# Kernel tuning notes

Hardware: AMD Instinct MI355X
Metric: run time of the kernel (lower is better)

## Reference

```python
import jax, jax.numpy as jnp
import numpy as np

N_ENT, N_REL, D = 20000, 500, 200
B, K = 8, 16


def setup_inputs() -> dict:
    key = jax.random.key(0)
    ks = jax.random.split(key, 24)
    inp = {}
    inp["batch"] = jax.random.randint(ks[0], (B, K, 3), 0, N_REL, dtype=jnp.int64 if jax.config.jax_enable_x64 else jnp.int32)
    inp["eemb"] = jax.random.normal(ks[1], (N_ENT, 2 * D), jnp.float32)
    inp["remb"] = jax.random.normal(ks[2], (N_REL, D), jnp.float32)
    inp["ce_re"] = jax.random.normal(ks[3], (N_ENT, D), jnp.float32)
    inp["ce_im"] = jax.random.normal(ks[4], (N_ENT, D), jnp.float32)
    inp["cr_re"] = jax.random.normal(ks[5], (N_REL, D), jnp.float32)
    inp["cr_im"] = jax.random.normal(ks[6], (N_REL, D), jnp.float32)
    inp["de"] = jax.random.normal(ks[7], (N_ENT, D), jnp.float32)
    inp["dr"] = jax.random.normal(ks[8], (N_REL, D), jnp.float32)
    inp["ke"] = jax.random.normal(ks[9], (N_ENT, D), jnp.float32)
    inp["kr"] = jax.random.normal(ks[10], (N_REL, D), jnp.float32)
    inp["se_h"] = jax.random.normal(ks[11], (N_ENT, D), jnp.float32)
    inp["se_t"] = jax.random.normal(ks[12], (N_ENT, D), jnp.float32)
    inp["sr"] = jax.random.normal(ks[13], (N_REL, D), jnp.float32)
    inp["sr_inv"] = jax.random.normal(ks[14], (N_REL, D), jnp.float32)
    # gate MLP params, stacked over 5 experts; uniform(0, 0.1) like cfg.model.init
    inp["W0"] = jax.random.uniform(ks[15], (5, 10, 64), jnp.float32) * 0.1
    inp["b0"] = jnp.zeros((5, 64), jnp.float32)
    inp["W1"] = jax.random.uniform(ks[16], (5, 64, 64), jnp.float32) * 0.1
    inp["b1"] = jnp.zeros((5, 64), jnp.float32)
    inp["W2"] = jax.random.uniform(ks[17], (5, 64, 64), jnp.float32) * 0.1
    inp["b2"] = jnp.zeros((5, 64), jnp.float32)
    inp["W3"] = jax.random.uniform(ks[18], (5, 64, 1), jnp.float32) * 0.1
    inp["b3"] = jnp.zeros((5, 1), jnp.float32)
    return inp


def _features_and_normalize(score):
    # min-max normalize per row, then summary features (eval mode: keep full row)
    mn = jnp.min(score, axis=1, keepdims=True)
    s = score - mn
    mx = jnp.max(s, axis=1, keepdims=True)
    s = s / mx
    mean = jnp.mean(s, axis=1, keepdims=True)
    var = jnp.var(s, axis=1, ddof=1, keepdims=True)  # torch.var default: unbiased
    return s, 1.0 - mean, var


def _forward(batch, eemb, remb, ce_re, ce_im, cr_re, cr_im, de, dr, ke, kr,
             se_h, se_t, sr, sr_inv, W0, b0, W1, b1, W2, b2, W3, b3):
    h = batch[:, 0, 0]  # h_index[:, 0]
    r = batch[:, 0, 2]  # r_index[:, 0]

    # --- RotatE: gather h, rotate by relation phase, broadcast diff vs full table
    d = remb.shape[1]
    he = eemb[h]                                  # [B, 2d]
    h_re, h_im = he[:, :d], he[:, d:]
    phase = remb[r]                               # [B, d]
    c, s_ = jnp.cos(phase), jnp.sin(phase)
    p_re = h_re * c - h_im * s_
    p_im = h_re * s_ + h_im * c
    t_re, t_im = eemb[:, :d], eemb[:, d:]         # [N, d]
    dre = p_re[:, None, :] - t_re[None]           # [B, N, d]
    dim = p_im[:, None, :] - t_im[None]
    rotate_score = -jnp.sqrt(dre * dre + dim * dim).sum(axis=-1)  # [B, N]

    # --- ComplEx: Re(<h, r, conj(t)>) against full table
    s_re = ce_re[h] * cr_re[r] - ce_im[h] * cr_im[r]
    s_im = ce_re[h] * cr_im[r] + ce_im[h] * cr_re[r]
    complex_score = s_re @ ce_re.T + s_im @ ce_im.T

    # --- KDG / DistMult / SimplE (bilinear diag scores vs full table)
    kdg_score = (ke[h] * kr[r]) @ ke.T
    distmult_score = (de[h] * dr[r]) @ de.T
    simple_score = 0.5 * ((se_h[h] * sr[r]) @ se_t.T + (se_t[h] * sr_inv[r]) @ se_h.T)

    scores, feats = [], []
    for sc in (rotate_score, complex_score, kdg_score, distmult_score, simple_score):
        ns, mdiffs, var = _features_and_normalize(sc)
        scores.append(ns)
        feats += [mdiffs, var]
    mlp_in = jnp.concatenate(feats, axis=1)       # [B, 10]

    # --- per-expert gate MLPs: Linear, Linear+ReLU, Linear+ReLU, Linear(1)+ReLU
    x = jnp.einsum('bi,eio->ebo', mlp_in, W0) + b0[:, None, :]
    x = jax.nn.relu(jnp.einsum('ebi,eio->ebo', x, W1) + b1[:, None, :])
    x = jax.nn.relu(jnp.einsum('ebi,eio->ebo', x, W2) + b2[:, None, :])
    w = jax.nn.relu(jnp.einsum('ebi,eio->ebo', x, W3) + b3[:, None, :])  # [5, B, 1]
    weights = w[:, :, 0].T                        # [B, 5]
    weights = weights / jnp.max(jnp.abs(weights), axis=1, keepdims=True)

    stacked = jnp.stack(scores, axis=1)           # [B, 5, N]
    return jnp.sum(weights[:, :, None] * stacked, axis=1)  # [B, N]


def reference(batch, eemb, remb, ce_re, ce_im, cr_re, cr_im, de, dr, ke, kr,
              se_h, se_t, sr, sr_inv, W0, b0, W1, b1, W2, b2, W3, b3):
    return _forward(batch, eemb, remb, ce_re, ce_im, cr_re, cr_im, de, dr, ke, kr,
                    se_h, se_t, sr, sr_inv, W0, b0, W1, b1, W2, b2, W3, b3)
```

## Files before the change

kernel.cpp:

```cpp
#include <hip/hip_runtime.h>
#include <math.h>

#define N_ENT 20000
#define D 200
#define NB 8
#define NM 5
#define NBLK_MAIN 1250

#define Q_OFF     0
#define PART_OFF  12800
#define MNMX_OFF  212800
#define STATD_OFF 212880
#define C_OFF     213040
#define CONST_OFF 213080
#define S_OFF     213088

#define COMP(v,j) ((j)==0 ? (v).x : (j)==1 ? (v).y : (j)==2 ? (v).z : (v).w)
#define LD4(p) (*(const float4*)(p))

__global__ __launch_bounds__(256) void k_q(
    const int* __restrict__ batch, const float* __restrict__ eemb,
    const float* __restrict__ remb,
    const float* __restrict__ ce_re, const float* __restrict__ ce_im,
    const float* __restrict__ cr_re, const float* __restrict__ cr_im,
    const float* __restrict__ de, const float* __restrict__ dr,
    const float* __restrict__ ke, const float* __restrict__ kr,
    const float* __restrict__ se_h, const float* __restrict__ se_t,
    const float* __restrict__ sr, const float* __restrict__ sr_inv,
    float* __restrict__ ws)
{
    int b = blockIdx.x;
    int d = threadIdx.x;
    if (d >= D) return;
    int h = batch[b*48 + 0];
    int r = batch[b*48 + 2];
    float* q = ws + Q_OFF;

    float her = eemb[h*400 + d];
    float hei = eemb[h*400 + 200 + d];
    float ph  = remb[r*200 + d];
    float cph = cosf(ph), sph = sinf(ph);
    q[(0*8 + b)*200 + d] = her*cph - hei*sph;
    q[(1*8 + b)*200 + d] = her*sph + hei*cph;

    float cer = ce_re[h*200+d], cei = ce_im[h*200+d];
    float crr = cr_re[r*200+d], cri = cr_im[r*200+d];
    q[(2*8 + b)*200 + d] = cer*crr - cei*cri;
    q[(3*8 + b)*200 + d] = cer*cri + cei*crr;

    q[(4*8 + b)*200 + d] = ke[h*200+d] * kr[r*200+d];
    q[(5*8 + b)*200 + d] = de[h*200+d] * dr[r*200+d];
    q[(6*8 + b)*200 + d] = se_h[h*200+d] * sr[r*200+d];
    q[(7*8 + b)*200 + d] = se_t[h*200+d] * sr_inv[r*200+d];
}

__global__ __launch_bounds__(256, 3) void k_main(
    const float* __restrict__ eemb, const float* __restrict__ ce_re,
    const float* __restrict__ ce_im, const float* __restrict__ ke,
    const float* __restrict__ de, const float* __restrict__ se_h,
    const float* __restrict__ se_t, float* __restrict__ ws)
{
    __shared__ __align__(16) float ebuf[2][8][16][32];
    __shared__ __align__(16) float qbuf[2][8][8][32];
    __shared__ float4 red2[2][40];

    const float* qg = ws + Q_OFF;
    float* S    = ws + S_OFF;
    float* part = ws + PART_OFF;

    const int tid = threadIdx.x;
    const int wv  = tid >> 6;
    const int l   = tid & 63;
    const int bg  = tid & 3;
    const int rg  = (tid >> 2) & 7;
    const int ds  = tid >> 5;
    const int e0  = blockIdx.x * 16;

    const float *gb0, *gb1; int gs0, go0, gs1, go1;
    switch (wv) {
        case 0: gb0 = eemb;  gs0 = 400; go0 = 0; gb1 = eemb;  gs1 = 400; go1 = 200; break;
        case 1: gb0 = ce_re; gs0 = 200; go0 = 0; gb1 = ce_im; gs1 = 200; go1 = 0;   break;
        case 2: gb0 = ke;    gs0 = 200; go0 = 0; gb1 = de;    gs1 = 200; go1 = 0;   break;
        default:gb0 = se_t;  gs0 = 200; go0 = 0; gb1 = se_h;  gs1 = 200; go1 = 0;   break;
    }
    const int sl = l & 7;
    const int rl = l >> 3;

    auto stage = [&](int buf, int c) {
#pragma unroll
        for (int a = 0; a < 2; ++a) {
            const float* gbase = a ? gb1 : gb0;
            const int gs_ = a ? gs1 : gs0, go_ = a ? go1 : go0;
#pragma unroll
            for (int i = 0; i < 2; ++i) {
                int rr  = i*8 + rl;
                int col = c*32 + ((sl ^ (rr & 7)) << 2);
                if (col + 4 > 200) col = 0;
                const float* gp = gbase + (size_t)(e0 + rr) * gs_ + go_ + col;
                float* lp = &ebuf[buf][2*wv + a][i*8][0];
                __builtin_amdgcn_global_load_lds(
                    (const __attribute__((address_space(1))) void*)gp,
                    (__attribute__((address_space(3))) void*)lp, 16, 0, 0);
            }
        }
#pragma unroll
        for (int a = 0; a < 2; ++a) {
            int v   = 2*wv + a;
            int col = c*32 + ((sl ^ rl) << 2);
            if (col + 4 > 200) col = 0;
            const float* gp = qg + (size_t)(v*8 + rl) * 200 + col;
            float* lp = &qbuf[buf][v][0][0];
            __builtin_amdgcn_global_load_lds(
                (const __attribute__((address_space(1))) void*)gp,
                (__attribute__((address_space(3))) void*)lp, 16, 0, 0);
        }
    };

    float acc[NM][2][2];
#pragma unroll
    for (int m = 0; m < NM; ++m)
#pragma unroll
        for (int je = 0; je < 2; ++je)
#pragma unroll
            for (int jb = 0; jb < 2; ++jb) acc[m][je][jb] = 0.f;

    const int eA = 2*rg, eB = 2*rg + 1;
    const int bA = 2*bg, bB = 2*bg + 1;
    const int peA = ((ds ^ (eA & 7)) << 2), peB = ((ds ^ (eB & 7)) << 2);
    const int pqA = ((ds ^ bA) << 2),       pqB = ((ds ^ bB) << 2);

    stage(0, 0);
    for (int c = 0; c < 7; ++c) {
        __syncthreads();
        if (c < 6) stage((c+1)&1, c+1);
        if (c*32 + ds*4 < 200) {
            const float* eb = &ebuf[c&1][0][0][0];
            const float* qb = &qbuf[c&1][0][0][0];
#define ELOAD(arr, pe, e) LD4(eb + (((arr)*16 + (e))*32) + (pe))
#define QLOAD(v, pq, b)   LD4(qb + (((v)*8 + (b))*32) + (pq))
            {
                float4 q0A=QLOAD(0,pqA,bA), q0B=QLOAD(0,pqB,bB);
                float4 q1A=QLOAD(1,pqA,bA), q1B=QLOAD(1,pqB,bB);
                float4 t0A=ELOAD(0,peA,eA), t0B=ELOAD(0,peB,eB);
                float4 t1A=ELOAD(1,peA,eA), t1B=ELOAD(1,peB,eB);
#pragma unroll
                for (int k = 0; k < 4; ++k) {
                    float dr_, di_;
                    dr_=COMP(q0A,k)-COMP(t0A,k); di_=COMP(q1A,k)-COMP(t1A,k);
                    acc[0][0][0] += __builtin_amdgcn_sqrtf(fmaf(dr_,dr_,di_*di_));
                    dr_=COMP(q0B,k)-COMP(t0A,k); di_=COMP(q1B,k)-COMP(t1A,k);
                    acc[0][0][1] += __builtin_amdgcn_sqrtf(fmaf(dr_,dr_,di_*di_));
                    dr_=COMP(q0A,k)-COMP(t0B,k); di_=COMP(q1A,k)-COMP(t1B,k);
                    acc[0][1][0] += __builtin_amdgcn_sqrtf(fmaf(dr_,dr_,di_*di_));
                    dr_=COMP(q0B,k)-COMP(t0B,k); di_=COMP(q1B,k)-COMP(t1B,k);
                    acc[0][1][1] += __builtin_amdgcn_sqrtf(fmaf(dr_,dr_,di_*di_));
                }
            }
            {
                float4 q2A=QLOAD(2,pqA,bA), q2B=QLOAD(2,pqB,bB);
                float4 q3A=QLOAD(3,pqA,bA), q3B=QLOAD(3,pqB,bB);
                float4 c0A=ELOAD(2,peA,eA), c0B=ELOAD(2,peB,eB);
                float4 c1A=ELOAD(3,peA,eA), c1B=ELOAD(3,peB,eB);
#pragma unroll
                for (int k = 0; k < 4; ++k) {
                    acc[1][0][0]=fmaf(COMP(q2A,k),COMP(c0A,k),fmaf(COMP(q3A,k),COMP(c1A,k),acc[1][0][0]));
                    acc[1][0][1]=fmaf(COMP(q2B,k),COMP(c0A,k),fmaf(COMP(q3B,k),COMP(c1A,k),acc[1][0][1]));
                    acc[1][1][0]=fmaf(COMP(q2A,k),COMP(c0B,k),fmaf(COMP(q3A,k),COMP(c1B,k),acc[1][1][0]));
                    acc[1][1][1]=fmaf(COMP(q2B,k),COMP(c0B,k),fmaf(COMP(q3B,k),COMP(c1B,k),acc[1][1][1]));
                }
            }
            {
                float4 q4A=QLOAD(4,pqA,bA), q4B=QLOAD(4,pqB,bB);
                float4 k0A=ELOAD(4,peA,eA), k0B=ELOAD(4,peB,eB);
                float4 q5A=QLOAD(5,pqA,bA), q5B=QLOAD(5,pqB,bB);
                float4 d0A=ELOAD(5,peA,eA), d0B=ELOAD(5,peB,eB);
#pragma unroll
                for (int k = 0; k < 4; ++k) {
                    acc[2][0][0]=fmaf(COMP(q4A,k),COMP(k0A,k),acc[2][0][0]);
                    acc[2][0][1]=fmaf(COMP(q4B,k),COMP(k0A,k),acc[2][0][1]);
                    acc[2][1][0]=fmaf(COMP(q4A,k),COMP(k0B,k),acc[2][1][0]);
                    acc[2][1][1]=fmaf(COMP(q4B,k),COMP(k0B,k),acc[2][1][1]);
                    acc[3][0][0]=fmaf(COMP(q5A,k),COMP(d0A,k),acc[3][0][0]);
                    acc[3][0][1]=fmaf(COMP(q5B,k),COMP(d0A,k),acc[3][0][1]);
                    acc[3][1][0]=fmaf(COMP(q5A,k),COMP(d0B,k),acc[3][1][0]);
                    acc[3][1][1]=fmaf(COMP(q5B,k),COMP(d0B,k),acc[3][1][1]);
                }
            }
            {
                float4 q6A=QLOAD(6,pqA,bA), q6B=QLOAD(6,pqB,bB);
                float4 q7A=QLOAD(7,pqA,bA), q7B=QLOAD(7,pqB,bB);
                float4 s0A=ELOAD(6,peA,eA), s0B=ELOAD(6,peB,eB);
                float4 s1A=ELOAD(7,peA,eA), s1B=ELOAD(7,peB,eB);
#pragma unroll
                for (int k = 0; k < 4; ++k) {
                    acc[4][0][0]=fmaf(COMP(q6A,k),COMP(s0A,k),fmaf(COMP(q7A,k),COMP(s1A,k),acc[4][0][0]));
                    acc[4][0][1]=fmaf(COMP(q6B,k),COMP(s0A,k),fmaf(COMP(q7B,k),COMP(s1A,k),acc[4][0][1]));
                    acc[4][1][0]=fmaf(COMP(q6A,k),COMP(s0B,k),fmaf(COMP(q7A,k),COMP(s1B,k),acc[4][1][0]));
                    acc[4][1][1]=fmaf(COMP(q6B,k),COMP(s0B,k),fmaf(COMP(q7B,k),COMP(s1B,k),acc[4][1][1]));
                }
            }
        }
    }

    __syncthreads();
    float* ov = &ebuf[0][0][0][0];
    {
        int base = tid * 20;
#pragma unroll
        for (int m = 0; m < NM; ++m)
#pragma unroll
            for (int je = 0; je < 2; ++je)
#pragma unroll
                for (int jb = 0; jb < 2; ++jb)
                    ov[base + m*4 + je*2 + jb] = acc[m][je][jb];
    }
    __syncthreads();
    if (tid < 128) {
        int e_l = tid >> 3, b = tid & 7;
        int rg2 = e_l >> 1, je = e_l & 1, bg2 = b >> 1, jb = b & 1;
        float vals[NM];
#pragma unroll
        for (int m = 0; m < NM; ++m) {
            float s = 0.f;
#pragma unroll
            for (int d2 = 0; d2 < 8; ++d2)
                s += ov[((d2 << 5) | (rg2 << 2) | bg2) * 20 + m*4 + je*2 + jb];
            vals[m] = s;
        }
        vals[0] = -vals[0];
        vals[4] = 0.5f * vals[4];
        int e = e0 + e_l;
#pragma unroll
        for (int m = 0; m < NM; ++m) S[(m*8 + b)*N_ENT + e] = vals[m];

        float mn[NM], mx[NM], sm[NM], sq[NM];
#pragma unroll
        for (int m = 0; m < NM; ++m) {
            mn[m] = vals[m]; mx[m] = vals[m]; sm[m] = vals[m]; sq[m] = vals[m]*vals[m];
        }
#pragma unroll
        for (int off = 8; off <= 32; off <<= 1) {
#pragma unroll
            for (int m = 0; m < NM; ++m) {
                mn[m] = fminf(mn[m], __shfl_xor(mn[m], off, 64));
                mx[m] = fmaxf(mx[m], __shfl_xor(mx[m], off, 64));
                sm[m] += __shfl_xor(sm[m], off, 64);
                sq[m] += __shfl_xor(sq[m], off, 64);
            }
        }
        if ((tid & 63) < 8) {
#pragma unroll
            for (int m = 0; m < NM; ++m)
                red2[tid >> 6][m*8 + b] = make_float4(mn[m], mx[m], sm[m], sq[m]);
        }
    }
    __syncthreads();
    if (tid < 40) {
        float4 u = red2[0][tid], v = red2[1][tid];
        float4 o;
        o.x = fminf(u.x, v.x);
        o.y = fmaxf(u.y, v.y);
        o.z = u.z + v.z;
        o.w = u.w + v.w;
        *(float4*)(part + (blockIdx.x*40 + tid)*4) = o;
    }
}

__global__ __launch_bounds__(256) void k_red(float* __restrict__ ws)
{
    const float* part = ws + PART_OFF;
    const int p = blockIdx.x;
    const int t = threadIdx.x;
    __shared__ float  smn[4], smx[4];
    __shared__ double ssm[4], ssq[4];

    float mn = INFINITY, mx = -INFINITY;
    double sm = 0.0, sq = 0.0;
    for (int blk = t; blk < NBLK_MAIN; blk += 256) {
        float4 v = LD4(part + (blk*40 + p)*4);
        mn = fminf(mn, v.x); mx = fmaxf(mx, v.y);
        sm += (double)v.z;   sq += (double)v.w;
    }
#pragma unroll
    for (int off = 1; off < 64; off <<= 1) {
        mn = fminf(mn, __shfl_xor(mn, off, 64));
        mx = fmaxf(mx, __shfl_xor(mx, off, 64));
        sm += __shfl_xor(sm, off, 64);
        sq += __shfl_xor(sq, off, 64);
    }
    if ((t & 63) == 0) {
        smn[t >> 6] = mn; smx[t >> 6] = mx; ssm[t >> 6] = sm; ssq[t >> 6] = sq;
    }
    __syncthreads();
    if (t == 0) {
        mn = fminf(fminf(smn[0], smn[1]), fminf(smn[2], smn[3]));
        mx = fmaxf(fmaxf(smx[0], smx[1]), fmaxf(smx[2], smx[3]));
        sm = ssm[0] + ssm[1] + ssm[2] + ssm[3];
        sq = ssq[0] + ssq[1] + ssq[2] + ssq[3];
        ws[MNMX_OFF + p*2]     = mn;
        ws[MNMX_OFF + p*2 + 1] = mx;
        double* sd = (double*)(ws + STATD_OFF);
        sd[p*2]     = sm;
        sd[p*2 + 1] = sq;
    }
}

__global__ __launch_bounds__(320) void k_mlp(
    const float* __restrict__ W0, const float* __restrict__ b0,
    const float* __restrict__ W1, const float* __restrict__ b1,
    const float* __restrict__ W2, const float* __restrict__ b2,
    const float* __restrict__ W3, const float* __restrict__ b3,
    float* __restrict__ ws)
{
    __shared__ float feat[NB][10];
    __shared__ float mnS[NM][NB], rngS[NM][NB];
    __shared__ float xA[NM][NB][64], xB[NM][NB][64];
    __shared__ float wS[NM][NB];

    int t = threadIdx.x;
    if (t < 40) {
        int m = t / 8, b = t % 8;
        float  mn = ws[MNMX_OFF + t*2];
        float  mx = ws[MNMX_OFF + t*2 + 1];
        const double* sd = (const double*)(ws + STATD_OFF);
        double sm = sd[t*2], sq = sd[t*2 + 1];
        float  rng  = mx - mn;
        double mean = sm / (double)N_ENT;
        float  md   = 1.0f - (float)((mean - (double)mn) / (double)rng);
        double va   = (sq - sm*sm/(double)N_ENT) / (double)(N_ENT - 1);
        float  vn   = (float)(va / ((double)rng * (double)rng));
        feat[b][2*m]   = md;
        feat[b][2*m+1] = vn;
        mnS[m][b] = mn; rngS[m][b] = rng;
    }
    __syncthreads();

    int ex = t / 64, o = t % 64;
    for (int b = 0; b < NB; ++b) {
        float a = b0[ex*64 + o];
#pragma unroll
        for (int i = 0; i < 10; ++i) a = fmaf(feat[b][i], W0[ex*640 + i*64 + o], a);
        xA[ex][b][o] = a;
    }
    __syncthreads();
    for (int b = 0; b < NB; ++b) {
        float a = b1[ex*64 + o];
        for (int i = 0; i < 64; ++i) a = fmaf(xA[ex][b][i], W1[ex*4096 + i*64 + o], a);
        xB[ex][b][o] = fmaxf(a, 0.f);
    }
    __syncthreads();
    for (int b = 0; b < NB; ++b) {
        float a = b2[ex*64 + o];
        for (int i = 0; i < 64; ++i) a = fmaf(xB[ex][b][i], W2[ex*4096 + i*64 + o], a);
        xA[ex][b][o] = fmaxf(a, 0.f);
    }
    __syncthreads();
    if (o == 0) {
        for (int b = 0; b < NB; ++b) {
            float a = b3[ex];
            for (int i = 0; i < 64; ++i) a = fmaf(xA[ex][b][i], W3[ex*64 + i], a);
            wS[ex][b] = fmaxf(a, 0.f);
        }
    }
    __syncthreads();
    if (t < 8) {
        int b = t;
        float wm = 0.f;
        for (int m = 0; m < NM; ++m) wm = fmaxf(wm, fabsf(wS[m][b]));
        float cst = 0.f;
        for (int m = 0; m < NM; ++m) {
            float w  = wS[m][b] / wm;
            float cc = w / rngS[m][b];
            ws[C_OFF + m*8 + b] = cc;
            cst -= cc * mnS[m][b];
        }
        ws[CONST_OFF + b] = cst;
    }
}

__global__ __launch_bounds__(256) void k_comb(const float* __restrict__ ws,
                                              float* __restrict__ out)
{
    int t = blockIdx.x * 256 + threadIdx.x;
    if (t >= NB * (N_ENT/4)) return;
    int b = t / (N_ENT/4);
    int e = (t % (N_ENT/4)) * 4;
    const float* S = ws + S_OFF;
    float c0 = ws[C_OFF +  0 + b], c1 = ws[C_OFF +  8 + b], c2 = ws[C_OFF + 16 + b];
    float c3 = ws[C_OFF + 24 + b], c4 = ws[C_OFF + 32 + b];
    float cst = ws[CONST_OFF + b];
    float4 s0 = *(const float4*)(S + (0*8 + b)*N_ENT + e);
    float4 s1 = *(const float4*)(S + (1*8 + b)*N_ENT + e);
    float4 s2 = *(const float4*)(S + (2*8 + b)*N_ENT + e);
    float4 s3 = *(const float4*)(S + (3*8 + b)*N_ENT + e);
    float4 s4 = *(const float4*)(S + (4*8 + b)*N_ENT + e);
    float4 o4;
    o4.x = fmaf(c0,s0.x, fmaf(c1,s1.x, fmaf(c2,s2.x, fmaf(c3,s3.x, fmaf(c4,s4.x, cst)))));
    o4.y = fmaf(c0,s0.y, fmaf(c1,s1.y, fmaf(c2,s2.y, fmaf(c3,s3.y, fmaf(c4,s4.y, cst)))));
    o4.z = fmaf(c0,s0.z, fmaf(c1,s1.z, fmaf(c2,s2.z, fmaf(c3,s3.z, fmaf(c4,s4.z, cst)))));
    o4.w = fmaf(c0,s0.w, fmaf(c1,s1.w, fmaf(c2,s2.w, fmaf(c3,s3.w, fmaf(c4,s4.w, cst)))));
    *(float4*)(out + b*N_ENT + e) = o4;
}

extern "C" void kernel_launch(void* const* d_in, const int* in_sizes, int n_in,
                              void* d_out, int out_size, void* d_ws, size_t ws_size,
                              hipStream_t stream)
{
    const int*   batch  = (const int*)  d_in[0];
    const float* eemb   = (const float*)d_in[1];
    const float* remb   = (const float*)d_in[2];
    const float* ce_re  = (const float*)d_in[3];
    const float* ce_im  = (const float*)d_in[4];
    const float* cr_re  = (const float*)d_in[5];
    const float* cr_im  = (const float*)d_in[6];
    const float* de     = (const float*)d_in[7];
    const float* dr     = (const float*)d_in[8];
    const float* ke     = (const float*)d_in[9];
    const float* kr     = (const float*)d_in[10];
    const float* se_h   = (const float*)d_in[11];
    const float* se_t   = (const float*)d_in[12];
    const float* sr     = (const float*)d_in[13];
    const float* sr_inv = (const float*)d_in[14];
    const float* W0 = (const float*)d_in[15];
    const float* b0 = (const float*)d_in[16];
    const float* W1 = (const float*)d_in[17];
    const float* b1 = (const float*)d_in[18];
    const float* W2 = (const float*)d_in[19];
    const float* b2 = (const float*)d_in[20];
    const float* W3 = (const float*)d_in[21];
    const float* b3 = (const float*)d_in[22];
    float* ws  = (float*)d_ws;
    float* out = (float*)d_out;

    k_q    <<<8, 256, 0, stream>>>(batch, eemb, remb, ce_re, ce_im, cr_re, cr_im,
                                   de, dr, ke, kr, se_h, se_t, sr, sr_inv, ws);
    k_main <<<NBLK_MAIN, 256, 0, stream>>>(eemb, ce_re, ce_im, ke, de, se_h, se_t, ws);
    k_red  <<<40, 256, 0, stream>>>(ws);
    k_mlp  <<<1, 320, 0, stream>>>(W0, b0, W1, b1, W2, b2, W3, b3, ws);
    k_comb <<<(NB*(N_ENT/4) + 255)/256, 256, 0, stream>>>(ws, out);
}
```

Before: 63.39 us.

## Load entity rows directly from global, stage only queries in LDS, wave-shuffle reductions

```diff
diff --git a/kernel.cpp b/kernel.cpp
--- a/kernel.cpp
+++ b/kernel.cpp
@@ -54,62 +54,38 @@
     q[(7*8 + b)*200 + d] = se_t[h*200+d] * sr_inv[r*200+d];
 }
 
-__global__ __launch_bounds__(256, 3) void k_main(
+__global__ __launch_bounds__(256, 4) void k_main(
     const float* __restrict__ eemb, const float* __restrict__ ce_re,
     const float* __restrict__ ce_im, const float* __restrict__ ke,
     const float* __restrict__ de, const float* __restrict__ se_h,
     const float* __restrict__ se_t, float* __restrict__ ws)
 {
-    __shared__ __align__(16) float ebuf[2][8][16][32];
-    __shared__ __align__(16) float qbuf[2][8][8][32];
-    __shared__ float4 red2[2][40];
+    __shared__ __align__(16) float qbuf[2][64][32];
 
     const float* qg = ws + Q_OFF;
     float* S    = ws + S_OFF;
     float* part = ws + PART_OFF;
 
     const int tid = threadIdx.x;
-    const int wv  = tid >> 6;
+    const int bg  = tid >> 6;
     const int l   = tid & 63;
-    const int bg  = tid & 3;
-    const int rg  = (tid >> 2) & 7;
-    const int ds  = tid >> 5;
+    const int ds  = (tid >> 3) & 7;
+    const int rg  = tid & 7;
     const int e0  = blockIdx.x * 16;
 
-    const float *gb0, *gb1; int gs0, go0, gs1, go1;
-    switch (wv) {
-        case 0: gb0 = eemb;  gs0 = 400; go0 = 0; gb1 = eemb;  gs1 = 400; go1 = 200; break;
-        case 1: gb0 = ce_re; gs0 = 200; go0 = 0; gb1 = ce_im; gs1 = 200; go1 = 0;   break;
-        case 2: gb0 = ke;    gs0 = 200; go0 = 0; gb1 = de;    gs1 = 200; go1 = 0;   break;
-        default:gb0 = se_t;  gs0 = 200; go0 = 0; gb1 = se_h;  gs1 = 200; go1 = 0;   break;
-    }
-    const int sl = l & 7;
-    const int rl = l >> 3;
-
-    auto stage = [&](int buf, int c) {
-#pragma unroll
-        for (int a = 0; a < 2; ++a) {
-            const float* gbase = a ? gb1 : gb0;
-            const int gs_ = a ? gs1 : gs0, go_ = a ? go1 : go0;
-#pragma unroll
-            for (int i = 0; i < 2; ++i) {
-                int rr  = i*8 + rl;
-                int col = c*32 + ((sl ^ (rr & 7)) << 2);
-                if (col + 4 > 200) col = 0;
-                const float* gp = gbase + (size_t)(e0 + rr) * gs_ + go_ + col;
-                float* lp = &ebuf[buf][2*wv + a][i*8][0];
-                __builtin_amdgcn_global_load_lds(
-                    (const __attribute__((address_space(1))) void*)gp,
-                    (__attribute__((address_space(3))) void*)lp, 16, 0, 0);
-            }
-        }
-#pragma unroll
-        for (int a = 0; a < 2; ++a) {
-            int v   = 2*wv + a;
-            int col = c*32 + ((sl ^ rl) << 2);
-            if (col + 4 > 200) col = 0;
-            const float* gp = qg + (size_t)(v*8 + rl) * 200 + col;
-            float* lp = &qbuf[buf][v][0][0];
+    const int eA = e0 + 2*rg, eB = eA + 1;
+    const int bA = 2*bg,      bB = bA + 1;
+
+    const int r0 = bg*16;
+    const int sr_ = l & 7;
+    const int rr_ = l >> 3;
+
+    auto stage_q = [&](int buf, int c) {
+#pragma unroll
+        for (int i = 0; i < 2; ++i) {
+            int row = r0 + i*8;
+            const float* gp = qg + (size_t)(row + rr_) * 200 + c*32 + (sr_ << 2);
+            float* lp = &qbuf[buf][row][0];
             __builtin_amdgcn_global_load_lds(
                 (const __attribute__((address_space(1))) void*)gp,
                 (__attribute__((address_space(3))) void*)lp, 16, 0, 0);
@@ -124,25 +100,22 @@
 #pragma unroll
             for (int jb = 0; jb < 2; ++jb) acc[m][je][jb] = 0.f;
 
-    const int eA = 2*rg, eB = 2*rg + 1;
-    const int bA = 2*bg, bB = 2*bg + 1;
-    const int peA = ((ds ^ (eA & 7)) << 2), peB = ((ds ^ (eB & 7)) << 2);
-    const int pqA = ((ds ^ bA) << 2),       pqB = ((ds ^ bB) << 2);
-
-    stage(0, 0);
+    stage_q(0, 0);
     for (int c = 0; c < 7; ++c) {
         __syncthreads();
-        if (c < 6) stage((c+1)&1, c+1);
-        if (c*32 + ds*4 < 200) {
-            const float* eb = &ebuf[c&1][0][0][0];
-            const float* qb = &qbuf[c&1][0][0][0];
-#define ELOAD(arr, pe, e) LD4(eb + (((arr)*16 + (e))*32) + (pe))
-#define QLOAD(v, pq, b)   LD4(qb + (((v)*8 + (b))*32) + (pq))
+        if (c < 6) stage_q((c+1)&1, c+1);
+        const int off = c*32 + ds*4;
+        if (off < 200) {
+            const float* qb = &qbuf[c&1][0][0];
+            const int dq = ds << 2;
+#define QLOAD(v, b)  LD4(qb + (((v)*8 + (b)) << 5) + dq)
             {
-                float4 q0A=QLOAD(0,pqA,bA), q0B=QLOAD(0,pqB,bB);
-                float4 q1A=QLOAD(1,pqA,bA), q1B=QLOAD(1,pqB,bB);
-                float4 t0A=ELOAD(0,peA,eA), t0B=ELOAD(0,peB,eB);
-                float4 t1A=ELOAD(1,peA,eA), t1B=ELOAD(1,peB,eB);
+                float4 q0A=QLOAD(0,bA), q0B=QLOAD(0,bB);
+                float4 q1A=QLOAD(1,bA), q1B=QLOAD(1,bB);
+                float4 t0A=LD4(eemb + (size_t)eA*400 + off);
+                float4 t0B=LD4(eemb + (size_t)eB*400 + off);
+                float4 t1A=LD4(eemb + (size_t)eA*400 + 200 + off);
+                float4 t1B=LD4(eemb + (size_t)eB*400 + 200 + off);
 #pragma unroll
                 for (int k = 0; k < 4; ++k) {
                     float dr_, di_;
@@ -157,10 +130,12 @@
                 }
             }
             {
-                float4 q2A=QLOAD(2,pqA,bA), q2B=QLOAD(2,pqB,bB);
-                float4 q3A=QLOAD(3,pqA,bA), q3B=QLOAD(3,pqB,bB);
-                float4 c0A=ELOAD(2,peA,eA), c0B=ELOAD(2,peB,eB);
-                float4 c1A=ELOAD(3,peA,eA), c1B=ELOAD(3,peB,eB);
+                float4 q2A=QLOAD(2,bA), q2B=QLOAD(2,bB);
+                float4 q3A=QLOAD(3,bA), q3B=QLOAD(3,bB);
+                float4 c0A=LD4(ce_re + (size_t)eA*200 + off);
+                float4 c0B=LD4(ce_re + (size_t)eB*200 + off);
+                float4 c1A=LD4(ce_im + (size_t)eA*200 + off);
+                float4 c1B=LD4(ce_im + (size_t)eB*200 + off);
 #pragma unroll
                 for (int k = 0; k < 4; ++k) {
                     acc[1][0][0]=fmaf(COMP(q2A,k),COMP(c0A,k),fmaf(COMP(q3A,k),COMP(c1A,k),acc[1][0][0]));
@@ -170,10 +145,12 @@
                 }
             }
             {
-                float4 q4A=QLOAD(4,pqA,bA), q4B=QLOAD(4,pqB,bB);
-                float4 k0A=ELOAD(4,peA,eA), k0B=ELOAD(4,peB,eB);
-                float4 q5A=QLOAD(5,pqA,bA), q5B=QLOAD(5,pqB,bB);
-                float4 d0A=ELOAD(5,peA,eA), d0B=ELOAD(5,peB,eB);
+                float4 q4A=QLOAD(4,bA), q4B=QLOAD(4,bB);
+                float4 k0A=LD4(ke + (size_t)eA*200 + off);
+                float4 k0B=LD4(ke + (size_t)eB*200 + off);
+                float4 q5A=QLOAD(5,bA), q5B=QLOAD(5,bB);
+                float4 d0A=LD4(de + (size_t)eA*200 + off);
+                float4 d0B=LD4(de + (size_t)eB*200 + off);
 #pragma unroll
                 for (int k = 0; k < 4; ++k) {
                     acc[2][0][0]=fmaf(COMP(q4A,k),COMP(k0A,k),acc[2][0][0]);
@@ -187,10 +164,12 @@
                 }
             }
             {
-                float4 q6A=QLOAD(6,pqA,bA), q6B=QLOAD(6,pqB,bB);
-                float4 q7A=QLOAD(7,pqA,bA), q7B=QLOAD(7,pqB,bB);
-                float4 s0A=ELOAD(6,peA,eA), s0B=ELOAD(6,peB,eB);
-                float4 s1A=ELOAD(7,peA,eA), s1B=ELOAD(7,peB,eB);
+                float4 q6A=QLOAD(6,bA), q6B=QLOAD(6,bB);
+                float4 s0A=LD4(se_t + (size_t)eA*200 + off);
+                float4 s0B=LD4(se_t + (size_t)eB*200 + off);
+                float4 q7A=QLOAD(7,bA), q7B=QLOAD(7,bB);
+                float4 s1A=LD4(se_h + (size_t)eA*200 + off);
+                float4 s1B=LD4(se_h + (size_t)eB*200 + off);
 #pragma unroll
                 for (int k = 0; k < 4; ++k) {
                     acc[4][0][0]=fmaf(COMP(q6A,k),COMP(s0A,k),fmaf(COMP(q7A,k),COMP(s1A,k),acc[4][0][0]));
@@ -202,67 +181,70 @@
         }
     }
 
-    __syncthreads();
-    float* ov = &ebuf[0][0][0][0];
-    {
-        int base = tid * 20;
+#pragma unroll
+    for (int off2 = 8; off2 <= 32; off2 <<= 1)
 #pragma unroll
         for (int m = 0; m < NM; ++m)
 #pragma unroll
             for (int je = 0; je < 2; ++je)
 #pragma unroll
                 for (int jb = 0; jb < 2; ++jb)
-                    ov[base + m*4 + je*2 + jb] = acc[m][je][jb];
-    }
-    __syncthreads();
-    if (tid < 128) {
-        int e_l = tid >> 3, b = tid & 7;
-        int rg2 = e_l >> 1, je = e_l & 1, bg2 = b >> 1, jb = b & 1;
-        float vals[NM];
-#pragma unroll
-        for (int m = 0; m < NM; ++m) {
-            float s = 0.f;
-#pragma unroll
-            for (int d2 = 0; d2 < 8; ++d2)
-                s += ov[((d2 << 5) | (rg2 << 2) | bg2) * 20 + m*4 + je*2 + jb];
-            vals[m] = s;
-        }
-        vals[0] = -vals[0];
-        vals[4] = 0.5f * vals[4];
-        int e = e0 + e_l;
-#pragma unroll
-        for (int m = 0; m < NM; ++m) S[(m*8 + b)*N_ENT + e] = vals[m];
-
-        float mn[NM], mx[NM], sm[NM], sq[NM];
-#pragma unroll
-        for (int m = 0; m < NM; ++m) {
-            mn[m] = vals[m]; mx[m] = vals[m]; sm[m] = vals[m]; sq[m] = vals[m]*vals[m];
-        }
-#pragma unroll
-        for (int off = 8; off <= 32; off <<= 1) {
-#pragma unroll
-            for (int m = 0; m < NM; ++m) {
-                mn[m] = fminf(mn[m], __shfl_xor(mn[m], off, 64));
-                mx[m] = fmaxf(mx[m], __shfl_xor(mx[m], off, 64));
-                sm[m] += __shfl_xor(sm[m], off, 64);
-                sq[m] += __shfl_xor(sq[m], off, 64);
-            }
-        }
-        if ((tid & 63) < 8) {
-#pragma unroll
-            for (int m = 0; m < NM; ++m)
-                red2[tid >> 6][m*8 + b] = make_float4(mn[m], mx[m], sm[m], sq[m]);
-        }
-    }
-    __syncthreads();
-    if (tid < 40) {
-        float4 u = red2[0][tid], v = red2[1][tid];
-        float4 o;
-        o.x = fminf(u.x, v.x);
-        o.y = fmaxf(u.y, v.y);
-        o.z = u.z + v.z;
-        o.w = u.w + v.w;
-        *(float4*)(part + (blockIdx.x*40 + tid)*4) = o;
+                    acc[m][je][jb] += __shfl_xor(acc[m][je][jb], off2, 64);
+
+    float vals[NM][2][2];
+#pragma unroll
+    for (int m = 0; m < NM; ++m)
+#pragma unroll
+        for (int je = 0; je < 2; ++je)
+#pragma unroll
+            for (int jb = 0; jb < 2; ++jb) {
+                float v = acc[m][je][jb];
+                if (m == 0) v = -v;
+                if (m == 4) v = 0.5f * v;
+                vals[m][je][jb] = v;
+            }
+
+#pragma unroll
+    for (int m = 0; m < NM; ++m) {
+        if (ds == m) {
+            S[(m*8 + bA)*N_ENT + eA] = vals[m][0][0];
+            S[(m*8 + bA)*N_ENT + eB] = vals[m][1][0];
+            S[(m*8 + bB)*N_ENT + eA] = vals[m][0][1];
+            S[(m*8 + bB)*N_ENT + eB] = vals[m][1][1];
+        }
+    }
+
+    float mn2[NM][2], mx2[NM][2], sm2[NM][2], sq2[NM][2];
+#pragma unroll
+    for (int m = 0; m < NM; ++m)
+#pragma unroll
+        for (int jb = 0; jb < 2; ++jb) {
+            float a = vals[m][0][jb], b = vals[m][1][jb];
+            mn2[m][jb] = fminf(a, b);
+            mx2[m][jb] = fmaxf(a, b);
+            sm2[m][jb] = a + b;
+            sq2[m][jb] = fmaf(a, a, b*b);
+        }
+#pragma unroll
+    for (int off2 = 1; off2 <= 4; off2 <<= 1)
+#pragma unroll
+        for (int m = 0; m < NM; ++m)
+#pragma unroll
+            for (int jb = 0; jb < 2; ++jb) {
+                mn2[m][jb] = fminf(mn2[m][jb], __shfl_xor(mn2[m][jb], off2, 64));
+                mx2[m][jb] = fmaxf(mx2[m][jb], __shfl_xor(mx2[m][jb], off2, 64));
+                sm2[m][jb] += __shfl_xor(sm2[m][jb], off2, 64);
+                sq2[m][jb] += __shfl_xor(sq2[m][jb], off2, 64);
+            }
+#pragma unroll
+    for (int m = 0; m < NM; ++m) {
+        if (ds == m && rg == 0) {
+#pragma unroll
+            for (int jb = 0; jb < 2; ++jb) {
+                float4 o = make_float4(mn2[m][jb], mx2[m][jb], sm2[m][jb], sq2[m][jb]);
+                *(float4*)(part + (blockIdx.x*40 + m*8 + bA + jb)*4) = o;
+            }
+        }
     }
 }
 
```

Result: slower. 89.30 us (+40.9%).

## Double entity tile per block to 32 with 512-thread blocks

Applied to the files above, without the earlier changes.

```diff
diff --git a/kernel.cpp b/kernel.cpp
--- a/kernel.cpp
+++ b/kernel.cpp
@@ -5,7 +5,7 @@
 #define D 200
 #define NB 8
 #define NM 5
-#define NBLK_MAIN 1250
+#define NBLK_MAIN 625
 
 #define Q_OFF     0
 #define PART_OFF  12800
@@ -54,15 +54,14 @@
     q[(7*8 + b)*200 + d] = se_t[h*200+d] * sr_inv[r*200+d];
 }
 
-__global__ __launch_bounds__(256, 3) void k_main(
+__global__ __launch_bounds__(512, 4) void k_main(
     const float* __restrict__ eemb, const float* __restrict__ ce_re,
     const float* __restrict__ ce_im, const float* __restrict__ ke,
     const float* __restrict__ de, const float* __restrict__ se_h,
     const float* __restrict__ se_t, float* __restrict__ ws)
 {
-    __shared__ __align__(16) float ebuf[2][8][16][32];
+    __shared__ __align__(16) float ebuf[2][8][32][32];
     __shared__ __align__(16) float qbuf[2][8][8][32];
-    __shared__ float4 red2[2][40];
 
     const float* qg = ws + Q_OFF;
     float* S    = ws + S_OFF;
@@ -72,44 +71,41 @@
     const int wv  = tid >> 6;
     const int l   = tid & 63;
     const int bg  = tid & 3;
-    const int rg  = (tid >> 2) & 7;
-    const int ds  = tid >> 5;
-    const int e0  = blockIdx.x * 16;
-
-    const float *gb0, *gb1; int gs0, go0, gs1, go1;
+    const int rg  = (tid >> 2) & 15;
+    const int ds  = wv;
+    const int e0  = blockIdx.x * 32;
+
+    const float* gb; int gs, go;
     switch (wv) {
-        case 0: gb0 = eemb;  gs0 = 400; go0 = 0; gb1 = eemb;  gs1 = 400; go1 = 200; break;
-        case 1: gb0 = ce_re; gs0 = 200; go0 = 0; gb1 = ce_im; gs1 = 200; go1 = 0;   break;
-        case 2: gb0 = ke;    gs0 = 200; go0 = 0; gb1 = de;    gs1 = 200; go1 = 0;   break;
-        default:gb0 = se_t;  gs0 = 200; go0 = 0; gb1 = se_h;  gs1 = 200; go1 = 0;   break;
+        case 0: gb = eemb;  gs = 400; go = 0;   break;
+        case 1: gb = eemb;  gs = 400; go = 200; break;
+        case 2: gb = ce_re; gs = 200; go = 0;   break;
+        case 3: gb = ce_im; gs = 200; go = 0;   break;
+        case 4: gb = ke;    gs = 200; go = 0;   break;
+        case 5: gb = de;    gs = 200; go = 0;   break;
+        case 6: gb = se_t;  gs = 200; go = 0;   break;
+        default:gb = se_h;  gs = 200; go = 0;   break;
     }
     const int sl = l & 7;
     const int rl = l >> 3;
 
     auto stage = [&](int buf, int c) {
 #pragma unroll
-        for (int a = 0; a < 2; ++a) {
-            const float* gbase = a ? gb1 : gb0;
-            const int gs_ = a ? gs1 : gs0, go_ = a ? go1 : go0;
-#pragma unroll
-            for (int i = 0; i < 2; ++i) {
-                int rr  = i*8 + rl;
-                int col = c*32 + ((sl ^ (rr & 7)) << 2);
-                if (col + 4 > 200) col = 0;
-                const float* gp = gbase + (size_t)(e0 + rr) * gs_ + go_ + col;
-                float* lp = &ebuf[buf][2*wv + a][i*8][0];
-                __builtin_amdgcn_global_load_lds(
-                    (const __attribute__((address_space(1))) void*)gp,
-                    (__attribute__((address_space(3))) void*)lp, 16, 0, 0);
-            }
-        }
-#pragma unroll
-        for (int a = 0; a < 2; ++a) {
-            int v   = 2*wv + a;
+        for (int i = 0; i < 4; ++i) {
+            int rr  = i*8 + rl;
+            int col = c*32 + ((sl ^ (rr & 7)) << 2);
+            if (col + 4 > 200) col = 0;
+            const float* gp = gb + (size_t)(e0 + rr) * gs + go + col;
+            float* lp = &ebuf[buf][wv][i*8][0];
+            __builtin_amdgcn_global_load_lds(
+                (const __attribute__((address_space(1))) void*)gp,
+                (__attribute__((address_space(3))) void*)lp, 16, 0, 0);
+        }
+        {
             int col = c*32 + ((sl ^ rl) << 2);
             if (col + 4 > 200) col = 0;
-            const float* gp = qg + (size_t)(v*8 + rl) * 200 + col;
-            float* lp = &qbuf[buf][v][0][0];
+            const float* gp = qg + (size_t)(wv*8 + rl) * 200 + col;
+            float* lp = &qbuf[buf][wv][0][0];
             __builtin_amdgcn_global_load_lds(
                 (const __attribute__((address_space(1))) void*)gp,
                 (__attribute__((address_space(3))) void*)lp, 16, 0, 0);
@@ -133,11 +129,12 @@
     for (int c = 0; c < 7; ++c) {
         __syncthreads();
         if (c < 6) stage((c+1)&1, c+1);
-        if (c*32 + ds*4 < 200) {
+        const int off = c*32 + ds*4;
+        if (off < 200) {
             const float* eb = &ebuf[c&1][0][0][0];
             const float* qb = &qbuf[c&1][0][0][0];
-#define ELOAD(arr, pe, e) LD4(eb + (((arr)*16 + (e))*32) + (pe))
-#define QLOAD(v, pq, b)   LD4(qb + (((v)*8 + (b))*32) + (pq))
+#define ELOAD(arr, pe, e) LD4(eb + (((arr)*32 + (e))*32) + (pe))
+#define QLOAD(v, pq, b)   LD4(qb + (((v)*8 + (b)) << 5) + (pq))
             {
                 float4 q0A=QLOAD(0,pqA,bA), q0B=QLOAD(0,pqB,bB);
                 float4 q1A=QLOAD(1,pqA,bA), q1B=QLOAD(1,pqB,bB);
@@ -215,7 +212,8 @@
                     ov[base + m*4 + je*2 + jb] = acc[m][je][jb];
     }
     __syncthreads();
-    if (tid < 128) {
+    float4* red2 = (float4*)&qbuf[0][0][0][0];
+    if (tid < 256) {
         int e_l = tid >> 3, b = tid & 7;
         int rg2 = e_l >> 1, je = e_l & 1, bg2 = b >> 1, jb = b & 1;
         float vals[NM];
@@ -224,7 +222,7 @@
             float s = 0.f;
 #pragma unroll
             for (int d2 = 0; d2 < 8; ++d2)
-                s += ov[((d2 << 5) | (rg2 << 2) | bg2) * 20 + m*4 + je*2 + jb];
+                s += ov[(d2*64 + rg2*4 + bg2) * 20 + m*4 + je*2 + jb];
             vals[m] = s;
         }
         vals[0] = -vals[0];
@@ -251,17 +249,20 @@
         if ((tid & 63) < 8) {
 #pragma unroll
             for (int m = 0; m < NM; ++m)
-                red2[tid >> 6][m*8 + b] = make_float4(mn[m], mx[m], sm[m], sq[m]);
+                red2[(tid >> 6)*40 + m*8 + b] = make_float4(mn[m], mx[m], sm[m], sq[m]);
         }
     }
     __syncthreads();
     if (tid < 40) {
-        float4 u = red2[0][tid], v = red2[1][tid];
-        float4 o;
-        o.x = fminf(u.x, v.x);
-        o.y = fmaxf(u.y, v.y);
-        o.z = u.z + v.z;
-        o.w = u.w + v.w;
+        float4 o = red2[tid];
+#pragma unroll
+        for (int w = 1; w < 4; ++w) {
+            float4 v = red2[w*40 + tid];
+            o.x = fminf(o.x, v.x);
+            o.y = fmaxf(o.y, v.y);
+            o.z += v.z;
+            o.w += v.w;
+        }
         *(float4*)(part + (blockIdx.x*40 + tid)*4) = o;
     }
 }
@@ -434,7 +435,7 @@
 
     k_q    <<<8, 256, 0, stream>>>(batch, eemb, remb, ce_re, ce_im, cr_re, cr_im,
                                    de, dr, ke, kr, se_h, se_t, sr, sr_inv, ws);
-    k_main <<<NBLK_MAIN, 256, 0, stream>>>(eemb, ce_re, ce_im, ke, de, se_h, se_t, ws);
+    k_main <<<NBLK_MAIN, 512, 0, stream>>>(eemb, ce_re, ce_im, ke, de, se_h, se_t, ws);
     k_red  <<<40, 256, 0, stream>>>(ws);
     k_mlp  <<<1, 320, 0, stream>>>(W0, b0, W1, b1, W2, b2, W3, b3, ws);
     k_comb <<<(NB*(N_ENT/4) + 255)/256, 256, 0, stream>>>(ws, out);
```

Result: slower. 68.02 us (+7.3%).
